# Performance work log

Measured on AMD Instinct MI355X. Metric: run time of the kernel, lower is better.

## Reference

```python
import jax, jax.numpy as jnp
import numpy as np

HEADS = 8
DIM_HEAD = 32
GSS = 3
SCALE = DIM_HEAD ** -0.5
LN_EPS = 1e-5


def setup_inputs() -> dict:
    key = jax.random.key(0)
    ks = jax.random.split(key, 5)
    B, C, H, W = 16, 256, 96, 96
    inner = HEADS * DIM_HEAD  # 256
    return {
        "x": jax.random.normal(ks[0], (B, C, H, W), jnp.float32),
        "w_qkv": jax.random.normal(ks[1], (inner * 3, C), jnp.float32) * 0.02,
        "group_tokens": jax.random.normal(ks[2], (C,), jnp.float32),
        "ln_gamma": jnp.ones((DIM_HEAD,), jnp.float32),
        "ln_beta": jnp.zeros((DIM_HEAD,), jnp.float32),
        "w_qk": jax.random.normal(ks[3], (inner * 2, inner), jnp.float32) * 0.02,
        "b_qk": jnp.zeros((inner * 2,), jnp.float32),
        "w_out": jax.random.normal(ks[4], (C, inner), jnp.float32) * 0.02,
        "b_out": jnp.zeros((C,), jnp.float32),
    }


def reference(x, w_qkv, group_tokens, ln_gamma, ln_beta, w_qk, b_qk, w_out, b_out):
    B, C, H, W = x.shape
    g, h, d = GSS, HEADS, DIM_HEAD
    X, Y = H // g, W // g
    n_groups = X * Y
    bg = B * n_groups
    win = g * g  # 9 tokens per spatial window

    # 'b c (h g1) (w g2) -> (b h w) c (g1 g2)'
    xg = x.reshape(B, C, X, g, Y, g).transpose(0, 2, 4, 1, 3, 5).reshape(bg, C, win)
    # prepend learned group token
    tok = jnp.broadcast_to(group_tokens[None, :, None], (bg, C, 1))
    xg = jnp.concatenate([tok, xg], axis=-1)

    # 1x1 conv QKV projection
    qkv = jnp.einsum('oc,bcn->bon', w_qkv, xg)
    q, k, v = jnp.split(qkv, 3, axis=1)

    def to_heads(t):  # 'b (h d) n -> b h n d'
        return t.reshape(bg, h, d, win + 1).transpose(0, 1, 3, 2)
    q, k, v = map(to_heads, (q, k, v))

    dots = jnp.einsum('bhid,bhjd->bhij', q * SCALE, k)
    attn = jax.nn.softmax(dots, axis=-1)
    out = jnp.einsum('bhij,bhjd->bhid', attn, v)

    gt = out[:, :, 0]    # [bg, h, d] group tokens
    gf = out[:, :, 1:]

    # '(b x y) h d -> b h (x y) d'
    gt = gt.reshape(B, n_groups, h, d).transpose(0, 2, 1, 3)
    # '(b x y) h n d -> b h (x y) n d'
    gf = gf.reshape(B, n_groups, h, win, d).transpose(0, 2, 1, 3, 4)

    # group_tokens_to_qk: LayerNorm(d) -> GELU -> 1x1 conv on (h d) channels
    mu = gt.mean(axis=-1, keepdims=True)
    var = gt.var(axis=-1, keepdims=True)
    gtn = (gt - mu) * jax.lax.rsqrt(var + LN_EPS) * ln_gamma + ln_beta
    gtn = jax.nn.gelu(gtn, approximate=False)
    # 'b h n c -> b (h c) n'
    t = gtn.transpose(0, 1, 3, 2).reshape(B, h * d, n_groups)
    qk = jnp.einsum('oc,bcn->bon', w_qk, t) + b_qk[None, :, None]
    # 'b (h c) n -> b h n c'
    qk = qk.reshape(B, h, 2 * d, n_groups).transpose(0, 1, 3, 2)
    w_q, w_k = jnp.split(qk, 2, axis=-1)

    # stage-2 hierarchical attention over group tokens
    w_dots = jnp.einsum('bhid,bhjd->bhij', w_q * SCALE, w_k)
    w_attn = jax.nn.softmax(w_dots, axis=-1)
    agg = jnp.einsum('bhij,bhjwd->bhiwd', w_attn, gf)

    # 'b h (x y) (g1 g2) d -> b (h d) (x g1) (y g2)'
    fmap = agg.reshape(B, h, X, Y, g, g, d).transpose(0, 1, 6, 2, 4, 3, 5)
    fmap = fmap.reshape(B, h * d, H, W)

    return jnp.einsum('oc,bchw->bohw', w_out, fmap) + b_out[None, :, None, None]
```

## Files before the change

### kernel.cpp

```cpp
#include <hip/hip_runtime.h>
#include <cmath>

namespace {
constexpr int kB  = 16;
constexpr int kNH = 8;
constexpr int kNG = 1024;
constexpr float kScale = 0.17677669529663687f;
}

typedef short  bf16x8 __attribute__((ext_vector_type(8)));
typedef short  bf16x4 __attribute__((ext_vector_type(4)));
typedef float  f32x4  __attribute__((ext_vector_type(4)));

__device__ __forceinline__ unsigned short f2b(float f) {
  unsigned int u = __builtin_bit_cast(unsigned int, f);
  u += 0x7fffu + ((u >> 16) & 1u);
  return (unsigned short)(u >> 16);
}
__device__ __forceinline__ float b2f(unsigned short h) {
  unsigned int u = ((unsigned int)h) << 16;
  return __builtin_bit_cast(float, u);
}

__global__ void __launch_bounds__(256) k_wcvt(const float* __restrict__ w_qkv,
                                              const float* __restrict__ w_out,
                                              unsigned short* __restrict__ wb,
                                              unsigned short* __restrict__ w_hi,
                                              unsigned short* __restrict__ w_lo) {
  int i = blockIdx.x * 256 + threadIdx.x;
  if (i < 196608) {
    wb[i] = f2b(w_qkv[i]);
  } else {
    int k = i - 196608;
    float v = w_out[k];
    unsigned short h = f2b(v);
    w_hi[k] = h;
    w_lo[k] = f2b(v - b2f(h));
  }
}

__global__ void __launch_bounds__(256, 2)
k_qkv_attn(const float* __restrict__ x, const unsigned short* __restrict__ w_bf,
           const float* __restrict__ gtok, const float* __restrict__ ln_g,
           const float* __restrict__ ln_b, unsigned short* __restrict__ t_b,
           unsigned short* __restrict__ gf_t) {
  __shared__ __align__(16) short smem[39680];
  short* qk_l = smem;
  short* vt   = smem + 16640;
  short* pl   = smem + 37120;

  const int tid = threadIdx.x;
  const int bid0 = blockIdx.x;
  const int lg  = (bid0 & 7) * 1024 + (bid0 >> 3);
  const int b   = lg >> 9;
  const int n0  = (lg & 511) * 2;
  const int wv  = tid >> 6;
  const int lane = tid & 63;
  const int ln  = lane & 15;
  const int qq  = lane >> 4;
  const int n0w = wv * 192;

  {
    const int m   = tid & 31;
    const int cw  = tid >> 5;
    const int m16 = m & 15;
    const float* srcp = nullptr;
    int strd = 0;
    if (m16 == 0) {
      srcp = gtok + cw; strd = 8;
    } else if (m16 <= 9) {
      int pix = m16 - 1;
      int n = n0 + (m >> 4);
      int gx = n >> 5, gy = n & 31;
      int gi = pix / 3, gj = pix - gi * 3;
      srcp = x + ((size_t)(b * 256 + cw) * 96 + gx * 3 + gi) * 96 + gy * 3 + gj;
      strd = 8 * 9216;
    }
    float vv[16];
#pragma unroll
    for (int half = 0; half < 2; ++half) {
#pragma unroll
      for (int r = 0; r < 16; ++r)
        vv[r] = srcp ? srcp[(size_t)(half * 16 + r) * strd] : 0.f;
#pragma unroll
      for (int r = 0; r < 16; ++r)
        qk_l[m * 264 + (half * 16 + r) * 8 + cw] = (short)f2b(vv[r]);
    }
  }
  __syncthreads();

  f32x4 acc[2][12];
#pragma unroll
  for (int mf = 0; mf < 2; ++mf)
#pragma unroll
    for (int nf = 0; nf < 12; ++nf) acc[mf][nf] = {0.f, 0.f, 0.f, 0.f};

  for (int ks = 0; ks < 8; ++ks) {
    bf16x8 a0 = *(const bf16x8*)&qk_l[ln * 264 + ks * 32 + qq * 8];
    bf16x8 a1 = *(const bf16x8*)&qk_l[(16 + ln) * 264 + ks * 32 + qq * 8];
#pragma unroll
    for (int nf = 0; nf < 12; ++nf) {
      bf16x8 bw = *(const bf16x8*)&w_bf[(size_t)(n0w + nf * 16 + ln) * 256 + ks * 32 + qq * 8];
      acc[0][nf] = __builtin_amdgcn_mfma_f32_16x16x32_bf16(a0, bw, acc[0][nf], 0, 0, 0);
      acc[1][nf] = __builtin_amdgcn_mfma_f32_16x16x32_bf16(a1, bw, acc[1][nf], 0, 0, 0);
    }
  }
  __syncthreads();

#pragma unroll
  for (int mf = 0; mf < 2; ++mf)
#pragma unroll
    for (int nf = 0; nf < 12; ++nf) {
      int o = n0w + nf * 16 + ln;
#pragma unroll
      for (int r = 0; r < 4; ++r) {
        short hv = (short)f2b(acc[mf][nf][r]);
        int ml = qq * 4 + r;
        if (o < 512) qk_l[(mf * 16 + ml) * 520 + o] = hv;
        else         vt[((mf << 8) + (o - 512)) * 40 + ml] = hv;
      }
    }
  for (int t = tid; t < 8192; t += 256) vt[(t >> 4) * 40 + 16 + (t & 15)] = 0;
  for (int t = tid; t < 1024; t += 256)
    pl[(t >> 8) * 640 + ((t & 255) >> 4) * 40 + 16 + (t & 15)] = 0;
  __syncthreads();

  for (int tt = 0; tt < 4; ++tt) {
    int task = wv * 4 + tt;
    int grp = task >> 3, hh = task & 7;
    int n = n0 + grp;

    bf16x8 aq = *(const bf16x8*)&qk_l[(grp * 16 + ln) * 520 + hh * 32 + qq * 8];
    bf16x8 bk = *(const bf16x8*)&qk_l[(grp * 16 + ln) * 520 + 256 + hh * 32 + qq * 8];
    f32x4 z = {0.f, 0.f, 0.f, 0.f};
    f32x4 s = __builtin_amdgcn_mfma_f32_16x16x32_bf16(aq, bk, z, 0, 0, 0);

    float pr[4], sm[4];
#pragma unroll
    for (int r = 0; r < 4; ++r) {
      float sv = s[r] * kScale;
      if (ln >= 10) sv = -1e30f;
      float mx = sv;
#pragma unroll
      for (int d = 1; d < 16; d <<= 1) mx = fmaxf(mx, __shfl_xor(mx, d));
      pr[r] = __expf(sv - mx);
      float t2 = pr[r];
#pragma unroll
      for (int d = 1; d < 16; d <<= 1) t2 += __shfl_xor(t2, d);
      sm[r] = t2;
    }
#pragma unroll
    for (int r = 0; r < 4; ++r)
      pl[wv * 640 + (qq * 4 + r) * 40 + ln] = (short)f2b(pr[r]);

    bf16x8 ap = *(const bf16x8*)&pl[wv * 640 + ln * 40 + qq * 8];
    bf16x8 v0 = *(const bf16x8*)&vt[((grp << 8) + hh * 32 + ln) * 40 + qq * 8];
    bf16x8 v1 = *(const bf16x8*)&vt[((grp << 8) + hh * 32 + 16 + ln) * 40 + qq * 8];
    f32x4 o0 = __builtin_amdgcn_mfma_f32_16x16x32_bf16(ap, v0, z, 0, 0, 0);
    f32x4 o1 = __builtin_amdgcn_mfma_f32_16x16x32_bf16(ap, v1, z, 0, 0, 0);

    if (qq == 0) {
      float inv0 = 1.f / sm[0];
      float va = o0[0] * inv0, vb = o1[0] * inv0;
      float ssum = va + vb;
#pragma unroll
      for (int d = 1; d < 16; d <<= 1) ssum += __shfl_xor(ssum, d);
      float mu = ssum * (1.f / 32.f);
      float dva = va - mu, dvb = vb - mu;
      float vsum = dva * dva + dvb * dvb;
#pragma unroll
      for (int d = 1; d < 16; d <<= 1) vsum += __shfl_xor(vsum, d);
      float ri = rsqrtf(vsum * (1.f / 32.f) + 1e-5f);
      float g0 = dva * ri * ln_g[ln] + ln_b[ln];
      float g1 = dvb * ri * ln_g[16 + ln] + ln_b[16 + ln];
      float e0 = 0.5f * g0 * (1.f + erff(g0 * 0.70710678118654752f));
      float e1 = 0.5f * g1 * (1.f + erff(g1 * 0.70710678118654752f));
      size_t tb = ((size_t)(b * 1024 + n)) * 256 + hh * 32 + ln;
      t_b[tb] = f2b(e0);
      t_b[tb + 16] = f2b(e1);
    }
#pragma unroll
    for (int r = 0; r < 4; ++r) {
      int i = qq * 4 + r;
      if (i >= 1 && i <= 9) {
        float inv = 1.f / sm[r];
        size_t base = ((size_t)((b * 8 + hh) * 288) + (i - 1) * 32 + ln) * 1024 + n;
        gf_t[base] = f2b(o0[r] * inv);
        gf_t[base + 16 * 1024] = f2b(o1[r] * inv);
      }
    }
  }
}

__global__ void __launch_bounds__(256, 2)
k_qk(const unsigned short* __restrict__ t_b, const float* __restrict__ w_qk,
     const float* __restrict__ b_qk, unsigned short* __restrict__ wq_b,
     unsigned short* __restrict__ wk_b) {
  __shared__ float t_l[128][33];
  __shared__ float w_l[64][33];
  int tid = threadIdx.x;
  int bid = blockIdx.x;
  int b = bid >> 6;
  int h = (bid >> 3) & 7;
  int nt = bid & 7;
  int n_base = nt * 128;
  int te = tid & 15, tn = tid >> 4;
  float accq[4][8] = {};
  for (int c0 = 0; c0 < 256; c0 += 32) {
    for (int i = 0; i < 16; ++i) {
      int nl = i * 8 + (tid >> 5);
      t_l[nl][tid & 31] = b2f(t_b[((size_t)(b * kNG) + n_base + nl) * 256 + c0 + (tid & 31)]);
    }
    for (int i = 0; i < 8; ++i) {
      int e = i * 8 + (tid >> 5);
      w_l[e][tid & 31] = w_qk[(size_t)(h * 64 + e) * 256 + c0 + (tid & 31)];
    }
    __syncthreads();
    for (int cc = 0; cc < 32; ++cc) {
      float wvv[4], tvv[8];
#pragma unroll
      for (int i = 0; i < 4; ++i) wvv[i] = w_l[te + 16 * i][cc];
#pragma unroll
      for (int j = 0; j < 8; ++j) tvv[j] = t_l[tn + 16 * j][cc];
#pragma unroll
      for (int i = 0; i < 4; ++i)
#pragma unroll
        for (int j = 0; j < 8; ++j) accq[i][j] += wvv[i] * tvv[j];
    }
    __syncthreads();
  }
#pragma unroll
  for (int i = 0; i < 4; ++i) {
    int e = te + 16 * i;
    float bias = b_qk[h * 64 + e];
#pragma unroll
    for (int j = 0; j < 8; ++j) {
      int n = n_base + tn + 16 * j;
      float v = accq[i][j] + bias;
      size_t idx = (((size_t)b * kNH + h) * kNG + n) * 32;
      if (e < 32) wq_b[idx + e] = f2b(v * kScale);
      else        wk_b[idx + (e - 32)] = f2b(v);
    }
  }
}

__global__ void __launch_bounds__(256, 3)
k_flash(const unsigned short* __restrict__ wq_b, const unsigned short* __restrict__ wk_b,
        const unsigned short* __restrict__ gf_t, unsigned short* __restrict__ agg_b) {
  __shared__ __align__(16) short vt[12800];
  __shared__ __align__(16) short pl[2560];
  __shared__ float al_l[64];
  __shared__ float lrow_l[64];

  const int tid = threadIdx.x;
  const int bid0 = blockIdx.x;
  const int xcd = bid0 & 7;
  const int s   = bid0 >> 3;
  const int bh  = xcd + 8 * (s >> 4);
  const int qt  = s & 15;
  const int wv = tid >> 6;
  const int lane = tid & 63;
  const int ln = lane & 15;
  const int qq = lane >> 4;
  const int d0 = wv * 80;

  bf16x8 aq = *(const bf16x8*)&wq_b[(size_t)(bh * 1024 + qt * 64 + wv * 16 + ln) * 32 + qq * 8];

  f32x4 accv[4][5];
  float mrow[4], lrow[4];
#pragma unroll
  for (int mf = 0; mf < 4; ++mf)
#pragma unroll
    for (int nf = 0; nf < 5; ++nf) accv[mf][nf] = {0.f, 0.f, 0.f, 0.f};
#pragma unroll
  for (int r = 0; r < 4; ++r) { mrow[r] = -1e30f; lrow[r] = 0.f; }

  for (int i = tid; i < 1280; i += 256) vt[11520 + i] = 0;

  for (int kt = 0; kt < 32; ++kt) {
    __syncthreads();
#pragma unroll
    for (int ii = 0; ii < 5; ++ii) {
      int i = ii * 256 + tid;
      if (i < 1152) {
        int d = i >> 2, c = (i & 3) * 8;
        bf16x8 g = *(const bf16x8*)&gf_t[((size_t)(bh * 288 + d)) * 1024 + kt * 32 + c];
        *(bf16x8*)&vt[d * 40 + c] = g;
      }
    }
    f32x4 z = {0.f, 0.f, 0.f, 0.f};
    bf16x8 kf0 = *(const bf16x8*)&wk_b[(size_t)(bh * 1024 + kt * 32 + ln) * 32 + qq * 8];
    bf16x8 kf1 = *(const bf16x8*)&wk_b[(size_t)(bh * 1024 + kt * 32 + 16 + ln) * 32 + qq * 8];
    f32x4 s0v = __builtin_amdgcn_mfma_f32_16x16x32_bf16(aq, kf0, z, 0, 0, 0);
    f32x4 s1v = __builtin_amdgcn_mfma_f32_16x16x32_bf16(aq, kf1, z, 0, 0, 0);
#pragma unroll
    for (int r = 0; r < 4; ++r) {
      float a0 = s0v[r], a1 = s1v[r];
      float tm = fmaxf(a0, a1);
#pragma unroll
      for (int d = 1; d < 16; d <<= 1) tm = fmaxf(tm, __shfl_xor(tm, d));
      float nm = fmaxf(mrow[r], tm);
      float al = __expf(mrow[r] - nm);
      mrow[r] = nm;
      float p0 = __expf(a0 - nm), p1 = __expf(a1 - nm);
      float ts = p0 + p1;
#pragma unroll
      for (int d = 1; d < 16; d <<= 1) ts += __shfl_xor(ts, d);
      lrow[r] = lrow[r] * al + ts;
      int row = wv * 16 + qq * 4 + r;
      pl[row * 40 + ln] = (short)f2b(p0);
      pl[row * 40 + 16 + ln] = (short)f2b(p1);
      if (ln == 0) al_l[row] = al;
    }
    __syncthreads();
#pragma unroll
    for (int mf = 0; mf < 4; ++mf)
#pragma unroll
      for (int r = 0; r < 4; ++r) {
        float alv = al_l[mf * 16 + qq * 4 + r];
#pragma unroll
        for (int nf = 0; nf < 5; ++nf) accv[mf][nf][r] *= alv;
      }
    bf16x8 ap[4];
#pragma unroll
    for (int mf = 0; mf < 4; ++mf)
      ap[mf] = *(const bf16x8*)&pl[(mf * 16 + ln) * 40 + qq * 8];
    __builtin_amdgcn_s_setprio(1);
#pragma unroll
    for (int nf = 0; nf < 5; ++nf) {
      bf16x8 vf = *(const bf16x8*)&vt[(d0 + nf * 16 + ln) * 40 + qq * 8];
#pragma unroll
      for (int mf = 0; mf < 4; ++mf)
        accv[mf][nf] = __builtin_amdgcn_mfma_f32_16x16x32_bf16(ap[mf], vf, accv[mf][nf], 0, 0, 0);
    }
    __builtin_amdgcn_s_setprio(0);
  }
#pragma unroll
  for (int r = 0; r < 4; ++r)
    if (ln == 0) lrow_l[wv * 16 + qq * 4 + r] = lrow[r];
  __syncthreads();
#pragma unroll
  for (int mf = 0; mf < 4; ++mf)
#pragma unroll
    for (int r = 0; r < 4; ++r) {
      float linv = 1.f / lrow_l[mf * 16 + qq * 4 + r];
      int row = qt * 64 + mf * 16 + qq * 4 + r;
#pragma unroll
      for (int nf = 0; nf < 5; ++nf) {
        int d = d0 + nf * 16 + ln;
        if (d < 288)
          agg_b[((size_t)(bh * 1024) + row) * 288 + d] = f2b(accv[mf][nf][r] * linv);
      }
    }
}

__global__ void __launch_bounds__(256, 2)
k_out(const unsigned short* __restrict__ agg_b,
      const unsigned short* __restrict__ w_hi, const unsigned short* __restrict__ w_lo,
      const float* __restrict__ b_out, float* __restrict__ out) {
  const int tid = threadIdx.x;
  const int bid = blockIdx.x;
  const int b = bid / 144;
  const int pt = bid - b * 144;
  const int p_base = pt * 64;
  const int wv = tid >> 6, lane = tid & 63, ln = lane & 15, qq = lane >> 4;
  const int obase = wv * 64;

  size_t vbase[4];
#pragma unroll
  for (int nf = 0; nf < 4; ++nf) {
    int p = p_base + nf * 16 + ln;
    int hh2 = p / 96, ww2 = p - hh2 * 96;
    int xg = hh2 / 3, gi = hh2 - xg * 3;
    int yg = ww2 / 3, gj = ww2 - yg * 3;
    int n = xg * 32 + yg, w = gi * 3 + gj;
    vbase[nf] = ((size_t)b * 8 * 1024 + n) * 288 + w * 32 + qq * 8;
  }

  f32x4 acc[4][4];
#pragma unroll
  for (int mf = 0; mf < 4; ++mf)
#pragma unroll
    for (int nf = 0; nf < 4; ++nf) acc[mf][nf] = {0.f, 0.f, 0.f, 0.f};

  for (int ks = 0; ks < 8; ++ks) {
    bf16x8 bfr[4];
#pragma unroll
    for (int nf = 0; nf < 4; ++nf)
      bfr[nf] = *(const bf16x8*)&agg_b[vbase[nf] + (size_t)ks * 294912];
#pragma unroll
    for (int mf = 0; mf < 4; ++mf) {
      int o = obase + mf * 16 + ln;
      bf16x8 ah = *(const bf16x8*)&w_hi[o * 256 + ks * 32 + qq * 8];
      bf16x8 al = *(const bf16x8*)&w_lo[o * 256 + ks * 32 + qq * 8];
#pragma unroll
      for (int nf = 0; nf < 4; ++nf) {
        acc[mf][nf] = __builtin_amdgcn_mfma_f32_16x16x32_bf16(ah, bfr[nf], acc[mf][nf], 0, 0, 0);
        acc[mf][nf] = __builtin_amdgcn_mfma_f32_16x16x32_bf16(al, bfr[nf], acc[mf][nf], 0, 0, 0);
      }
    }
  }
#pragma unroll
  for (int mf = 0; mf < 4; ++mf) {
#pragma unroll
    for (int r = 0; r < 4; ++r) {
      int o = obase + mf * 16 + qq * 4 + r;
      float bias = b_out[o];
#pragma unroll
      for (int nf = 0; nf < 4; ++nf) {
        int p = p_base + nf * 16 + ln;
        out[((size_t)b * 256 + o) * 9216 + p] = acc[mf][nf][r] + bias;
      }
    }
  }
}

extern "C" void kernel_launch(void* const* d_in, const int* in_sizes, int n_in,
                              void* d_out, int out_size, void* d_ws, size_t ws_size,
                              hipStream_t stream) {
  const float* x     = (const float*)d_in[0];
  const float* w_qkv = (const float*)d_in[1];
  const float* gtok  = (const float*)d_in[2];
  const float* ln_g  = (const float*)d_in[3];
  const float* ln_b  = (const float*)d_in[4];
  const float* w_qk  = (const float*)d_in[5];
  const float* b_qk  = (const float*)d_in[6];
  const float* w_out = (const float*)d_in[7];
  const float* b_out = (const float*)d_in[8];
  float* out = (float*)d_out;

  unsigned short* ws   = (unsigned short*)d_ws;
  unsigned short* w_bf = ws;
  unsigned short* t_b  = w_bf + 196608;
  unsigned short* wq_b = t_b + 4194304;
  unsigned short* wk_b = wq_b + 4194304;
  unsigned short* gf_t = wk_b + 4194304;
  unsigned short* agg_b = gf_t + 37748736;
  unsigned short* w_hi = agg_b + 37748736;
  unsigned short* w_lo = w_hi + 65536;

  k_wcvt<<<1024, 256, 0, stream>>>(w_qkv, w_out, w_bf, w_hi, w_lo);
  k_qkv_attn<<<8192, 256, 0, stream>>>(x, w_bf, gtok, ln_g, ln_b, t_b, gf_t);
  k_qk<<<1024, 256, 0, stream>>>(t_b, w_qk, b_qk, wq_b, wk_b);
  k_flash<<<2048, 256, 0, stream>>>(wq_b, wk_b, gf_t, agg_b);
  k_out<<<2304, 256, 0, stream>>>(agg_b, w_hi, w_lo, b_out, out);
}
```

Baseline: 1.314 ms.

## Split fused QKV-attention kernel into transpose, dense QKV GEMM, and attention kernels

Replaces the fused per-window kernel, which gathered strided x pixels and did a small GEMM per block, with three stages. The stages are a bf16 transpose of x into pixel-major layout, a tiled 128x128 MFMA GEMM producing QKV for all pixels, and an attention kernel that reads Q/K/V from global memory. The group-token projection is computed once in a tiny kernel instead of once per window, and V is staged in LDS with an XOR swizzle to avoid bank conflicts. Batches are processed in chunks sized to the workspace. This adds a large intermediate round trip through HBM and more launches in exchange for better GEMM efficiency and coalesced loads.

Result: faster. 1.256 ms (-4.4%).

```diff
diff --git a/kernel.cpp b/kernel.cpp
--- a/kernel.cpp
+++ b/kernel.cpp
@@ -2,7 +2,6 @@
 #include <cmath>
 
 namespace {
-constexpr int kB  = 16;
 constexpr int kNH = 8;
 constexpr int kNG = 1024;
 constexpr float kScale = 0.17677669529663687f;
@@ -20,6 +19,9 @@
 __device__ __forceinline__ float b2f(unsigned short h) {
   unsigned int u = ((unsigned int)h) << 16;
   return __builtin_bit_cast(float, u);
+}
+__device__ __forceinline__ int swc(int row, int col) {
+  return col ^ (((row >> 3) & 3) << 3);
 }
 
 __global__ void __launch_bounds__(256) k_wcvt(const float* __restrict__ w_qkv,
@@ -39,100 +41,160 @@
   }
 }
 
+__global__ void __launch_bounds__(256) k_tok(const float* __restrict__ w_qkv,
+                                             const float* __restrict__ gtok,
+                                             unsigned short* __restrict__ tok_b) {
+  int o = blockIdx.x * 256 + threadIdx.x;
+  if (o < 768) {
+    float s = 0.f;
+    for (int c = 0; c < 256; ++c) s += w_qkv[o * 256 + c] * gtok[c];
+    tok_b[o] = f2b(s);
+  }
+}
+
 __global__ void __launch_bounds__(256, 2)
-k_qkv_attn(const float* __restrict__ x, const unsigned short* __restrict__ w_bf,
-           const float* __restrict__ gtok, const float* __restrict__ ln_g,
-           const float* __restrict__ ln_b, unsigned short* __restrict__ t_b,
-           unsigned short* __restrict__ gf_t) {
-  __shared__ __align__(16) short smem[39680];
-  short* qk_l = smem;
-  short* vt   = smem + 16640;
-  short* pl   = smem + 37120;
-
+k_xt(const float* __restrict__ x, unsigned short* __restrict__ xt, int b0) {
+  __shared__ short Lt[64][72];
   const int tid = threadIdx.x;
-  const int bid0 = blockIdx.x;
-  const int lg  = (bid0 & 7) * 1024 + (bid0 >> 3);
-  const int b   = lg >> 9;
-  const int n0  = (lg & 511) * 2;
-  const int wv  = tid >> 6;
-  const int lane = tid & 63;
-  const int ln  = lane & 15;
-  const int qq  = lane >> 4;
-  const int n0w = wv * 192;
+  const int bid = blockIdx.x;
+  const int bb = bid / 576;
+  const int r2 = bid - bb * 576;
+  const int ct = r2 / 144;
+  const int ptile = r2 - ct * 144;
+  const int c0 = ct * 64, p0 = ptile * 64;
+  const float* xb = x + ((size_t)((b0 + bb) * 256 + c0)) * 9216 + p0;
+#pragma unroll
+  for (int i = 0; i < 16; ++i) {
+    int idx = i * 256 + tid;
+    int c = idx >> 6, p = idx & 63;
+    Lt[c][p] = (short)f2b(xb[(size_t)c * 9216 + p]);
+  }
+  __syncthreads();
+  unsigned short* xto = xt + ((size_t)bb * 9216 + p0) * 256 + c0;
+#pragma unroll
+  for (int i = 0; i < 2; ++i) {
+    int t = i * 256 + tid;
+    int p = t & 63, oc = t >> 6;
+    bf16x8 v8;
+#pragma unroll
+    for (int e = 0; e < 8; ++e) v8[e] = Lt[oc * 8 + e][p];
+    *(bf16x8*)&xto[(size_t)p * 256 + oc * 8] = v8;
+  }
+}
+
+__global__ void __launch_bounds__(256, 4)
+k_qkv(const unsigned short* __restrict__ w_bf, const unsigned short* __restrict__ xt,
+      unsigned short* __restrict__ qkv) {
+  const int tid = threadIdx.x;
+  const int N = gridDim.x;
+  const int lg = (blockIdx.x & 7) * (N >> 3) + (blockIdx.x >> 3);
+  const int pt = lg / 6;
+  const int ot = lg - pt * 6;
+  const int o0 = ot * 128;
+  const int wv = tid >> 6, lane = tid & 63, ln = lane & 15, qq = lane >> 4;
+  const int ow = (wv >> 1) * 64, pw = (wv & 1) * 64;
+  const size_t prow = (size_t)pt * 128 + pw;
+  const unsigned short* xbase = xt + (prow + ln) * 256;
+  const unsigned short* wbase = w_bf + (size_t)(o0 + ow + ln) * 256;
+
+  f32x4 acc[4][4];
+#pragma unroll
+  for (int mf = 0; mf < 4; ++mf)
+#pragma unroll
+    for (int nf = 0; nf < 4; ++nf) acc[mf][nf] = {0.f, 0.f, 0.f, 0.f};
+
+  for (int ks = 0; ks < 8; ++ks) {
+    const int co = ks * 32 + qq * 8;
+    bf16x8 bfr[4], afr[4];
+#pragma unroll
+    for (int nf = 0; nf < 4; ++nf) bfr[nf] = *(const bf16x8*)&xbase[(size_t)nf * 4096 + co];
+#pragma unroll
+    for (int mf = 0; mf < 4; ++mf) afr[mf] = *(const bf16x8*)&wbase[(size_t)mf * 4096 + co];
+#pragma unroll
+    for (int mf = 0; mf < 4; ++mf)
+#pragma unroll
+      for (int nf = 0; nf < 4; ++nf)
+        acc[mf][nf] = __builtin_amdgcn_mfma_f32_16x16x32_bf16(afr[mf], bfr[nf], acc[mf][nf], 0, 0, 0);
+  }
+#pragma unroll
+  for (int mf = 0; mf < 4; ++mf)
+#pragma unroll
+    for (int nf = 0; nf < 4; ++nf) {
+      bf16x4 sv;
+#pragma unroll
+      for (int r = 0; r < 4; ++r) sv[r] = (short)f2b(acc[mf][nf][r]);
+      *(bf16x4*)&qkv[(prow + nf * 16 + ln) * 768 + o0 + ow + mf * 16 + qq * 4] = sv;
+    }
+}
+
+__global__ void __launch_bounds__(256, 3)
+k_attn(const unsigned short* __restrict__ qkv, const unsigned short* __restrict__ tok_b,
+       const float* __restrict__ ln_g, const float* __restrict__ ln_b,
+       unsigned short* __restrict__ t_b, unsigned short* __restrict__ gf_t, int b0) {
+  __shared__ __align__(16) short smem[23040];
+  short* vt = smem;
+  short* pl = smem + 20480;
+
+  const int tid = threadIdx.x;
+  const int N = gridDim.x;
+  const int lg = (blockIdx.x & 7) * (N >> 3) + (blockIdx.x >> 3);
+  const int bb = lg >> 9;
+  const int b  = b0 + bb;
+  const int n0 = (lg & 511) * 2;
+  const int wv = tid >> 6, lane = tid & 63, ln = lane & 15, qq = lane >> 4;
+  const int grp = wv >> 1;
+  const int n = n0 + grp;
+  const size_t brow = (size_t)bb * 9216;
 
   {
-    const int m   = tid & 31;
-    const int cw  = tid >> 5;
-    const int m16 = m & 15;
-    const float* srcp = nullptr;
-    int strd = 0;
-    if (m16 == 0) {
-      srcp = gtok + cw; strd = 8;
-    } else if (m16 <= 9) {
-      int pix = m16 - 1;
-      int n = n0 + (m >> 4);
-      int gx = n >> 5, gy = n & 31;
-      int gi = pix / 3, gj = pix - gi * 3;
-      srcp = x + ((size_t)(b * 256 + cw) * 96 + gx * 3 + gi) * 96 + gy * 3 + gj;
-      strd = 8 * 9216;
-    }
-    float vv[16];
-#pragma unroll
-    for (int half = 0; half < 2; ++half) {
-#pragma unroll
-      for (int r = 0; r < 16; ++r)
-        vv[r] = srcp ? srcp[(size_t)(half * 16 + r) * strd] : 0.f;
-#pragma unroll
-      for (int r = 0; r < 16; ++r)
-        qk_l[m * 264 + (half * 16 + r) * 8 + cw] = (short)f2b(vv[r]);
+    bf16x8 z8 = {0, 0, 0, 0, 0, 0, 0, 0};
+    for (int i = 0; i < 12; ++i) {
+      int off = (i * 256 + tid) * 8;
+      if (off < 23040) *(bf16x8*)&smem[off] = z8;
     }
   }
   __syncthreads();
 
-  f32x4 acc[2][12];
-#pragma unroll
-  for (int mf = 0; mf < 2; ++mf)
-#pragma unroll
-    for (int nf = 0; nf < 12; ++nf) acc[mf][nf] = {0.f, 0.f, 0.f, 0.f};
-
-  for (int ks = 0; ks < 8; ++ks) {
-    bf16x8 a0 = *(const bf16x8*)&qk_l[ln * 264 + ks * 32 + qq * 8];
-    bf16x8 a1 = *(const bf16x8*)&qk_l[(16 + ln) * 264 + ks * 32 + qq * 8];
-#pragma unroll
-    for (int nf = 0; nf < 12; ++nf) {
-      bf16x8 bw = *(const bf16x8*)&w_bf[(size_t)(n0w + nf * 16 + ln) * 256 + ks * 32 + qq * 8];
-      acc[0][nf] = __builtin_amdgcn_mfma_f32_16x16x32_bf16(a0, bw, acc[0][nf], 0, 0, 0);
-      acc[1][nf] = __builtin_amdgcn_mfma_f32_16x16x32_bf16(a1, bw, acc[1][nf], 0, 0, 0);
-    }
+  for (int it = 0; it < 9; ++it) {
+    int t = it * 256 + tid;
+    if (t < 2304) {
+      int win = t >= 1152 ? 1 : 0;
+      int rem = t - win * 1152;
+      int pix = rem >> 7, dp = rem & 127, d = dp * 2;
+      int nn = n0 + win;
+      int gx = nn >> 5, gy = nn & 31;
+      int gi = (pix * 11) >> 5, gj = pix - 3 * gi;
+      int p = (gx * 3 + gi) * 96 + gy * 3 + gj;
+      unsigned int u = *(const unsigned int*)&qkv[(brow + p) * 768 + 512 + d];
+      int col = pix + 1;
+      int r0 = (win << 8) + d;
+      vt[r0 * 40 + swc(r0, col)] = (short)(u & 0xffffu);
+      vt[(r0 + 1) * 40 + swc(r0 + 1, col)] = (short)(u >> 16);
+    }
+  }
+#pragma unroll
+  for (int i = 0; i < 2; ++i) {
+    int t = i * 256 + tid;
+    vt[t * 40 + swc(t, 0)] = (short)tok_b[512 + (t & 255)];
   }
   __syncthreads();
 
-#pragma unroll
-  for (int mf = 0; mf < 2; ++mf)
-#pragma unroll
-    for (int nf = 0; nf < 12; ++nf) {
-      int o = n0w + nf * 16 + ln;
-#pragma unroll
-      for (int r = 0; r < 4; ++r) {
-        short hv = (short)f2b(acc[mf][nf][r]);
-        int ml = qq * 4 + r;
-        if (o < 512) qk_l[(mf * 16 + ml) * 520 + o] = hv;
-        else         vt[((mf << 8) + (o - 512)) * 40 + ml] = hv;
-      }
-    }
-  for (int t = tid; t < 8192; t += 256) vt[(t >> 4) * 40 + 16 + (t & 15)] = 0;
-  for (int t = tid; t < 1024; t += 256)
-    pl[(t >> 8) * 640 + ((t & 255) >> 4) * 40 + 16 + (t & 15)] = 0;
-  __syncthreads();
-
+  const unsigned short* rowq;
+  {
+    bool isPix = (ln >= 1 && ln <= 9);
+    int pix = ln - 1;
+    int gi = isPix ? ((pix * 11) >> 5) : 0;
+    int gj = isPix ? (pix - 3 * gi) : 0;
+    int gx = n >> 5, gy = n & 31;
+    int p = (gx * 3 + gi) * 96 + gy * 3 + gj;
+    rowq = isPix ? qkv + (brow + p) * 768 + qq * 8 : tok_b + qq * 8;
+  }
+
+  f32x4 z = {0.f, 0.f, 0.f, 0.f};
   for (int tt = 0; tt < 4; ++tt) {
-    int task = wv * 4 + tt;
-    int grp = task >> 3, hh = task & 7;
-    int n = n0 + grp;
-
-    bf16x8 aq = *(const bf16x8*)&qk_l[(grp * 16 + ln) * 520 + hh * 32 + qq * 8];
-    bf16x8 bk = *(const bf16x8*)&qk_l[(grp * 16 + ln) * 520 + 256 + hh * 32 + qq * 8];
-    f32x4 z = {0.f, 0.f, 0.f, 0.f};
+    int hh = (wv & 1) * 4 + tt;
+    bf16x8 aq = *(const bf16x8*)&rowq[hh * 32];
+    bf16x8 bk = *(const bf16x8*)&rowq[256 + hh * 32];
     f32x4 s = __builtin_amdgcn_mfma_f32_16x16x32_bf16(aq, bk, z, 0, 0, 0);
 
     float pr[4], sm[4];
@@ -154,8 +216,10 @@
       pl[wv * 640 + (qq * 4 + r) * 40 + ln] = (short)f2b(pr[r]);
 
     bf16x8 ap = *(const bf16x8*)&pl[wv * 640 + ln * 40 + qq * 8];
-    bf16x8 v0 = *(const bf16x8*)&vt[((grp << 8) + hh * 32 + ln) * 40 + qq * 8];
-    bf16x8 v1 = *(const bf16x8*)&vt[((grp << 8) + hh * 32 + 16 + ln) * 40 + qq * 8];
+    int rv0 = (grp << 8) + hh * 32 + ln;
+    int rv1 = rv0 + 16;
+    bf16x8 v0 = *(const bf16x8*)&vt[rv0 * 40 + swc(rv0, qq * 8)];
+    bf16x8 v1 = *(const bf16x8*)&vt[rv1 * 40 + swc(rv1, qq * 8)];
     f32x4 o0 = __builtin_amdgcn_mfma_f32_16x16x32_bf16(ap, v0, z, 0, 0, 0);
     f32x4 o1 = __builtin_amdgcn_mfma_f32_16x16x32_bf16(ap, v1, z, 0, 0, 0);
 
@@ -373,8 +437,8 @@
     int hh2 = p / 96, ww2 = p - hh2 * 96;
     int xg = hh2 / 3, gi = hh2 - xg * 3;
     int yg = ww2 / 3, gj = ww2 - yg * 3;
-    int n = xg * 32 + yg, w = gi * 3 + gj;
-    vbase[nf] = ((size_t)b * 8 * 1024 + n) * 288 + w * 32 + qq * 8;
+    int nn = xg * 32 + yg, w = gi * 3 + gj;
+    vbase[nf] = ((size_t)b * 8 * 1024 + nn) * 288 + w * 32 + qq * 8;
   }
 
   f32x4 acc[4][4];
@@ -431,16 +495,36 @@
 
   unsigned short* ws   = (unsigned short*)d_ws;
   unsigned short* w_bf = ws;
-  unsigned short* t_b  = w_bf + 196608;
-  unsigned short* wq_b = t_b + 4194304;
-  unsigned short* wk_b = wq_b + 4194304;
-  unsigned short* gf_t = wk_b + 4194304;
-  unsigned short* agg_b = gf_t + 37748736;
-  unsigned short* w_hi = agg_b + 37748736;
-  unsigned short* w_lo = w_hi + 65536;
+  unsigned short* w_hi = ws + 196608;
+  unsigned short* w_lo = ws + 262144;
+  unsigned short* tok  = ws + 327680;
+  unsigned short* t_b  = ws + 328704;
+  unsigned short* wq_b = ws + 4523008;
+  unsigned short* wk_b = ws + 8717312;
+  unsigned short* gf_t = ws + 12911616;
+  unsigned short* R    = ws + 50660352;
+
+  auto need = [](int NBv) -> size_t {
+    size_t reg = (size_t)NBv * 9437184ull;
+    if (reg < 37748736ull) reg = 37748736ull;
+    return (50660352ull + reg) * 2ull;
+  };
+  int NB = 4;
+  if (ws_size >= need(16)) NB = 16;
+  else if (ws_size >= need(8)) NB = 8;
+
+  unsigned short* qkv = R;
+  unsigned short* xt  = R + (size_t)NB * 7077888ull;
+  unsigned short* agg_b = R;
 
   k_wcvt<<<1024, 256, 0, stream>>>(w_qkv, w_out, w_bf, w_hi, w_lo);
-  k_qkv_attn<<<8192, 256, 0, stream>>>(x, w_bf, gtok, ln_g, ln_b, t_b, gf_t);
+  k_tok<<<3, 256, 0, stream>>>(w_qkv, gtok, tok);
+  for (int c = 0; c < 16 / NB; ++c) {
+    int b0 = c * NB;
+    k_xt<<<NB * 576, 256, 0, stream>>>(x, xt, b0);
+    k_qkv<<<NB * 432, 256, 0, stream>>>(w_bf, xt, qkv);
+    k_attn<<<NB * 512, 256, 0, stream>>>(qkv, tok, ln_g, ln_b, t_b, gf_t, b0);
+  }
   k_qk<<<1024, 256, 0, stream>>>(t_b, w_qk, b_qk, wq_b, wk_b);
   k_flash<<<2048, 256, 0, stream>>>(wq_b, wk_b, gf_t, agg_b);
   k_out<<<2304, 256, 0, stream>>>(agg_b, w_hi, w_lo, b_out, out);
```
